# Kernel optimization log

Hardware: AMD Instinct MI355X
Metric: run time of the kernel (lower is better)

## Reference

```python
import jax, jax.numpy as jnp
import numpy as np

N_AC, N_W, D_IN = 40000, 20000, 128
H, DH, D_OUT = 4, 64, 64
E_TIC, E_W, E_REL = 400000, 200000, 400000
NEG = 0.2  # DGL GATConv leaky_relu negative slope


def _edge_softmax(e, dst, n_dst):
    # e: (E, H) edge logits; softmax over edges sharing the same dst node
    m = jax.ops.segment_max(e, dst, num_segments=n_dst)
    m = jnp.where(jnp.isfinite(m), m, 0.0)
    ex = jnp.exp(e - m[dst])
    s = jax.ops.segment_sum(ex, dst, num_segments=n_dst)
    return ex / (s[dst] + 1e-9)


def _gat(x_src, x_dst, src, dst, ew, W, al, ar, b, n_dst, act):
    # DGL GATConv (eval mode: dropouts are identity). al/ar: (H, D)
    Hh, Dd = al.shape
    z_src = (x_src @ W).reshape(-1, Hh, Dd)
    z_dst = (x_dst @ W).reshape(-1, Hh, Dd)
    el = jnp.einsum('nhd,hd->nh', z_src, al)
    er = jnp.einsum('nhd,hd->nh', z_dst, ar)
    e = jax.nn.leaky_relu(el[src] + er[dst], NEG)              # (E, H)
    a = _edge_softmax(e, dst, n_dst) * ew[:, None]             # attention * edge_weight
    out = jax.ops.segment_sum(z_src[src] * a[:, :, None], dst, num_segments=n_dst)
    out = out + b.reshape(1, Hh, Dd)
    return act(out) if act is not None else out


def _forward(x_ac, x_w, w_tic, w_w, w_rel,
             W1_tic, al1_tic, ar1_tic, b1_tic,
             W1_w, al1_w, ar1_w, b1_w,
             W1_rel, al1_rel, ar1_rel, b1_rel,
             W2_tic, al2_tic, ar2_tic, b2_tic,
             W2_w, al2_w, ar2_w, b2_w,
             W2_rel, al2_rel, ar2_rel, b2_rel,
             src_tic, dst_tic, src_w, dst_w, src_rel, dst_rel):
    elu = jax.nn.elu
    # --- layer 1 (H=4 heads, ELU activation inside GATConv) ---
    h_tic = _gat(x_ac, x_ac, src_tic, dst_tic, w_tic, W1_tic, al1_tic, ar1_tic, b1_tic, N_AC, elu)
    h_w1 = _gat(x_w, x_w, src_w, dst_w, w_w, W1_w, al1_w, ar1_w, b1_w, N_W, elu)
    h_rel = _gat(x_ac, x_w, src_rel, dst_rel, w_rel, W1_rel, al1_rel, ar1_rel, b1_rel, N_W, elu)
    # HeteroGraphConv aggregate='mean' over etypes per dst node type, flatten heads, ReLU
    h_ac = jax.nn.relu(h_tic.reshape(N_AC, -1))
    h_word = jax.nn.relu(((h_w1 + h_rel) * 0.5).reshape(N_W, -1))
    # --- layer 2 (single head, no activation) ---
    o_tic = _gat(h_ac, h_ac, src_tic, dst_tic, w_tic, W2_tic, al2_tic, ar2_tic, b2_tic, N_AC, None)
    o_w = _gat(h_word, h_word, src_w, dst_w, w_w, W2_w, al2_w, ar2_w, b2_w, N_W, None)
    o_rel = _gat(h_ac, h_word, src_rel, dst_rel, w_rel, W2_rel, al2_rel, ar2_rel, b2_rel, N_W, None)
    return (o_tic.reshape(N_AC, -1), ((o_w + o_rel) * 0.5).reshape(N_W, -1))


def setup_inputs() -> dict:
    key = jax.random.key(0)
    ks = iter(jax.random.split(key, 48))
    def p(shape):
        return jax.random.normal(next(ks), shape, jnp.float32) * 0.05
    inp = {
        'x_ac': jax.random.normal(next(ks), (N_AC, D_IN), jnp.float32),
        'x_w': jax.random.normal(next(ks), (N_W, D_IN), jnp.float32),
        'w_tic': jax.random.uniform(next(ks), (E_TIC,), jnp.float32),
        'w_w': jax.random.uniform(next(ks), (E_W,), jnp.float32),
        'w_rel': jax.random.uniform(next(ks), (E_REL,), jnp.float32),
    }
    # per-etype GATConv params: layer1 (H heads), layer2 (1 head)
    for name, fin, h, d in [('1_tic', D_IN, H, DH), ('1_w', D_IN, H, DH), ('1_rel', D_IN, H, DH),
                            ('2_tic', H * DH, 1, D_OUT), ('2_w', H * DH, 1, D_OUT), ('2_rel', H * DH, 1, D_OUT)]:
        inp['W' + name] = p((fin, h * d))
        inp['al' + name] = p((h, d))
        inp['ar' + name] = p((h, d))
        inp['b' + name] = p((h * d,))
    inp['src_tic'] = jax.random.randint(next(ks), (E_TIC,), 0, N_AC, jnp.int32)
    inp['dst_tic'] = jax.random.randint(next(ks), (E_TIC,), 0, N_AC, jnp.int32)
    inp['src_w'] = jax.random.randint(next(ks), (E_W,), 0, N_W, jnp.int32)
    inp['dst_w'] = jax.random.randint(next(ks), (E_W,), 0, N_W, jnp.int32)
    inp['src_rel'] = jax.random.randint(next(ks), (E_REL,), 0, N_AC, jnp.int32)
    inp['dst_rel'] = jax.random.randint(next(ks), (E_REL,), 0, N_W, jnp.int32)
    return inp


def reference(x_ac, x_w, w_tic, w_w, w_rel,
              W1_tic, al1_tic, ar1_tic, b1_tic,
              W1_w, al1_w, ar1_w, b1_w,
              W1_rel, al1_rel, ar1_rel, b1_rel,
              W2_tic, al2_tic, ar2_tic, b2_tic,
              W2_w, al2_w, ar2_w, b2_w,
              W2_rel, al2_rel, ar2_rel, b2_rel,
              src_tic, dst_tic, src_w, dst_w, src_rel, dst_rel):
    return _forward(x_ac, x_w, w_tic, w_w, w_rel,
                    W1_tic, al1_tic, ar1_tic, b1_tic,
                    W1_w, al1_w, ar1_w, b1_w,
                    W1_rel, al1_rel, ar1_rel, b1_rel,
                    W2_tic, al2_tic, ar2_tic, b2_tic,
                    W2_w, al2_w, ar2_w, b2_w,
                    W2_rel, al2_rel, ar2_rel, b2_rel,
                    src_tic, dst_tic, src_w, dst_w, src_rel, dst_rel)
```

## Files before the change

### kernel.cpp

```cpp
#include <hip/hip_runtime.h>
#include <hip/hip_bf16.h>

typedef unsigned short ushort_t;
typedef __attribute__((ext_vector_type(8))) short bf16x8;
typedef __attribute__((ext_vector_type(4))) float f32x4;

#define N_AC 40000
#define N_W  20000
#define D_IN 128
#define NH   4
#define HD   256
#define DOUT 64
#define E_TIC 400000
#define E_W   200000
#define E_REL 400000
#define E_ALL 1000000
#define N_ALL 80000
#define NEG 0.2f
#define CAP 96
#define FCH 4096
#define ELLW 64

__device__ __forceinline__ float bf2f(ushort_t u) {
    return __uint_as_float(((unsigned int)u) << 16);
}
__device__ __forceinline__ ushort_t f2bf(float v) {
    unsigned u = __float_as_uint(v);
    unsigned r = (u + 0x7fffu + ((u >> 16) & 1u)) >> 16;
    return (ushort_t)r;
}
__device__ __forceinline__ float ldf(const void* p, size_t i, int f) {
    return f ? ((const float*)p)[i] : bf2f(((const ushort_t*)p)[i]);
}
__device__ __forceinline__ float lrelu_exp(float v) {
    v = v > 0.f ? v : NEG * v;
    return __expf(v);
}

__global__ void detect_dtype(const ushort_t* __restrict__ x, int* __restrict__ flag) {
    __shared__ int hit;
    if (threadIdx.x == 0) hit = 0;
    __syncthreads();
    for (int i = threadIdx.x; i < 4096; i += 256) {
        float v = bf2f(x[i]);
        if (!(fabsf(v) <= 1e4f)) atomicOr(&hit, 1);
    }
    __syncthreads();
    if (threadIdx.x == 0) flag[0] = hit ? 1 : 0;
}

struct CvtTab { const void* src[24]; int n[24]; int off[24]; };
__global__ __launch_bounds__(256) void cvt_inputs(CvtTab t, float* __restrict__ par,
                                                  const int* __restrict__ flagp) {
    int ent = blockIdx.x >> 3, sub = blockIdx.x & 7;
    int f = flagp[0];
    const void* s = t.src[ent];
    int n = t.n[ent];
    float* d = par + t.off[ent];
    for (int i = sub * 256 + threadIdx.x; i < n; i += 8 * 256)
        d[i] = f ? ((const float*)s)[i] : bf2f(((const ushort_t*)s)[i]);
}

struct QTab { int woff[2]; int aoff[2]; int qoff[2]; int K[2]; int Hh[2]; };
__global__ __launch_bounds__(256) void make_q(QTab t, float* __restrict__ par) {
    int b = blockIdx.x;
    int k = threadIdx.x;
    int K = t.K[b], Hh = t.Hh[b];
    if (k >= K) return;
    const float* W = par + t.woff[b];
    const float* a = par + t.aoff[b];
    float* q = par + t.qoff[b];
    int HDc = Hh * 64;
    for (int h = 0; h < Hh; ++h) {
        float s = 0.f;
        for (int d = 0; d < 64; ++d) s += W[(size_t)k * HDc + h * 64 + d] * a[h * 64 + d];
        q[k * Hh + h] = s;
    }
}

struct PTab { int woff[6]; int toff[6]; int Klog[6]; int N[6]; };
__global__ __launch_bounds__(256) void pack_wt(PTab t, const float* __restrict__ par,
                                               ushort_t* __restrict__ wt) {
    int m = blockIdx.x >> 4, sub = blockIdx.x & 15;
    int Klog = t.Klog[m], K = 1 << Klog, Nn = t.N[m];
    int tot = K * Nn;
    const float* Wp = par + t.woff[m];
    ushort_t* d = wt + t.toff[m];
    for (int i = sub * 256 + threadIdx.x; i < tot; i += 16 * 256) {
        int n = i >> Klog, k = i & (K - 1);
        d[i] = f2bf(Wp[(size_t)k * Nn + n]);
    }
}


__device__ __forceinline__ void dev_mgemm1(int b, const void* X, int f,
                                           const ushort_t* WT, ushort_t* Zb,
                                           const float* alp, const float* arp,
                                           float* elo, float* ero) {
    const int w = threadIdx.x >> 6, l = threadIdx.x & 63;
    const int row0 = b * 16;
    const int lr = l & 15, lk = l >> 4;

    bf16x8 a[4];
    if (!f) {
        const ushort_t* xp = (const ushort_t*)X + (size_t)(row0 + lr) * 128 + lk * 8;
        #pragma unroll
        for (int ks = 0; ks < 4; ++ks) a[ks] = *(const bf16x8*)(xp + ks * 32);
    } else {
        const float* xp = (const float*)X + (size_t)(row0 + lr) * 128 + lk * 8;
        #pragma unroll
        for (int ks = 0; ks < 4; ++ks)
            #pragma unroll
            for (int j = 0; j < 8; ++j) a[ks][j] = (short)f2bf(xp[ks * 32 + j]);
    }

    f32x4 acc[4] = {{0.f,0.f,0.f,0.f},{0.f,0.f,0.f,0.f},{0.f,0.f,0.f,0.f},{0.f,0.f,0.f,0.f}};
    const int col0 = w * 64;
    #pragma unroll
    for (int ks = 0; ks < 4; ++ks) {
        #pragma unroll
        for (int nt = 0; nt < 4; ++nt) {
            bf16x8 bb = *(const bf16x8*)(WT + (size_t)(col0 + nt * 16 + lr) * 128 + ks * 32 + lk * 8);
            acc[nt] = __builtin_amdgcn_mfma_f32_16x16x32_bf16(a[ks], bb, acc[nt], 0, 0, 0);
        }
    }
    #pragma unroll
    for (int nt = 0; nt < 4; ++nt)
        #pragma unroll
        for (int r = 0; r < 4; ++r)
            Zb[(size_t)(row0 + lk * 4 + r) * HD + col0 + nt * 16 + lr] = f2bf(acc[nt][r]);

    if (alp) {
        float a0 = alp[col0 + lr], a1 = alp[col0 + 16 + lr],
              a2 = alp[col0 + 32 + lr], a3 = alp[col0 + 48 + lr];
        #pragma unroll
        for (int r = 0; r < 4; ++r) {
            float v = acc[0][r] * a0 + acc[1][r] * a1 + acc[2][r] * a2 + acc[3][r] * a3;
            v += __shfl_xor(v, 1, 64); v += __shfl_xor(v, 2, 64);
            v += __shfl_xor(v, 4, 64); v += __shfl_xor(v, 8, 64);
            if (lr == r) elo[(size_t)(row0 + lk * 4 + r) * 4 + w] = v;
        }
    }
    if (arp) {
        float a0 = arp[col0 + lr], a1 = arp[col0 + 16 + lr],
              a2 = arp[col0 + 32 + lr], a3 = arp[col0 + 48 + lr];
        #pragma unroll
        for (int r = 0; r < 4; ++r) {
            float v = acc[0][r] * a0 + acc[1][r] * a1 + acc[2][r] * a2 + acc[3][r] * a3;
            v += __shfl_xor(v, 1, 64); v += __shfl_xor(v, 2, 64);
            v += __shfl_xor(v, 4, 64); v += __shfl_xor(v, 8, 64);
            if (lr == r) ero[(size_t)(row0 + lk * 4 + r) * 4 + w] = v;
        }
    }
}

__device__ __forceinline__ void dev_fill_ell(int b,
        const int* s0, const int* d0, const void* w0,
        const int* s1, const int* d1, const void* w1,
        const int* s2, const int* d2, const void* w2,
        int f, int* cnt, unsigned* adj) {
    const int CB[9] = {0, 12500, 25000, 37500, 50000, 61250, 67500, 73750, 80000};
    const int cls = b & 7;
    const int lo = CB[cls], hi = CB[cls + 1];
    const int e0 = (b >> 3) * FCH;
    for (int i = threadIdx.x; i < FCH; i += 256) {
        int e = e0 + i;
        if (e >= E_ALL) return;
        int g;
        if (e < E_TIC) g = d0[e];
        else if (e < E_TIC + E_W) g = N_AC + d1[e - E_TIC];
        else g = N_AC + N_W + d2[e - E_TIC - E_W];
        if (g < lo || g >= hi) continue;
        int sn; float ew;
        if (e < E_TIC) { sn = s0[e]; ew = ldf(w0, e, f); }
        else if (e < E_TIC + E_W) { int le = e - E_TIC; sn = s1[le]; ew = ldf(w1, le, f); }
        else { int le = e - E_TIC - E_W; sn = s2[le]; ew = ldf(w2, le, f); }
        int r = atomicAdd(&cnt[g], 1);
        if (r < ELLW)
            adj[(size_t)g * ELLW + r] = (unsigned)(sn & 0xFFFF) | ((unsigned)f2bf(ew) << 16);
    }
}

__device__ __forceinline__ void dev_elr1(int b, const void* X, int f,
                                         const float* q0, float* o0,
                                         int N, int D, int Hh) {
    __shared__ float qs[512];
    const int tid = threadIdx.x;
    const int tot = D * Hh;
    for (int i = tid; i < tot; i += 256) {
        int k, h;
        if (Hh == 4) { k = i >> 2; h = i & 3; } else { k = i; h = 0; }
        qs[h * D + k] = q0[i];
    }
    __syncthreads();
    const int wid = tid >> 6, lane = tid & 63;
    const int n = b * 4 + wid;
    if (n >= N) return;
    const int J = D >> 6;
    float x[4];
    for (int j = 0; j < J; ++j) x[j] = ldf(X, (size_t)n * D + j * 64 + lane, f);
    for (int h = 0; h < Hh; ++h) {
        float v = 0.f;
        for (int j = 0; j < J; ++j) v += x[j] * qs[h * D + j * 64 + lane];
        #pragma unroll
        for (int o = 32; o > 0; o >>= 1) v += __shfl_down(v, o, 64);
        if (lane == 0) o0[n * Hh + h] = v;
    }
}

struct FA {
    const int *s0, *d0; const void* w0;
    const int *s1, *d1; const void* w1;
    const int *s2, *d2; const void* w2;
    const int* flagp; int* cnt; unsigned* adj;
    const void* x_ac; const void* x_w;
    const ushort_t *WTt, *WTw, *WTr;
    ushort_t *Zt, *Zw, *Zr;
    const float *al1t, *ar1t, *al1w, *ar1w, *al1r;
    float *ELt, *ERt, *ELw, *ERw, *ELr, *ERr;
    const float* qer1r;
    unsigned c0, c1, c2, c3;
};
__global__ __launch_bounds__(256) void fused_a(FA a) {
    const unsigned b = blockIdx.x;
    const int f = a.flagp[0];
    if (b < a.c0) {
        dev_fill_ell(b, a.s0, a.d0, a.w0, a.s1, a.d1, a.w1, a.s2, a.d2, a.w2,
                     f, a.cnt, a.adj);
    } else if (b < a.c1) {
        dev_mgemm1(b - a.c0, a.x_ac, f, a.WTt, a.Zt, a.al1t, a.ar1t, a.ELt, a.ERt);
    } else if (b < a.c2) {
        dev_mgemm1(b - a.c1, a.x_w, f, a.WTw, a.Zw, a.al1w, a.ar1w, a.ELw, a.ERw);
    } else if (b < a.c3) {
        dev_mgemm1(b - a.c2, a.x_ac, f, a.WTr, a.Zr, a.al1r, nullptr, a.ELr, nullptr);
    } else {
        dev_elr1(b - a.c3, a.x_w, f, a.qer1r, a.ERr, N_W, 128, 4);
    }
}

__global__ __launch_bounds__(256) void count3(const int* __restrict__ d0,
                                              const int* __restrict__ d1,
                                              const int* __restrict__ d2,
                                              int* __restrict__ cnt,
                                              int* __restrict__ rank) {
    int e = blockIdx.x * 256 + threadIdx.x;
    if (e >= E_ALL) return;
    int g;
    if (e < E_TIC) g = d0[e];
    else if (e < E_TIC + E_W) g = N_AC + d1[e - E_TIC];
    else g = N_AC + N_W + d2[e - E_TIC - E_W];
    rank[e] = atomicAdd(&cnt[g], 1);
}

__global__ __launch_bounds__(256) void scan_bsum(const int* __restrict__ cnt,
                                                 int* __restrict__ bsum, int N) {
    __shared__ int red[256];
    int i = blockIdx.x * 256 + threadIdx.x;
    red[threadIdx.x] = (i < N) ? cnt[i] : 0;
    __syncthreads();
    #pragma unroll
    for (int o = 128; o > 0; o >>= 1) {
        if (threadIdx.x < o) red[threadIdx.x] += red[threadIdx.x + o];
        __syncthreads();
    }
    if (threadIdx.x == 0) bsum[blockIdx.x] = red[0];
}

__global__ __launch_bounds__(512) void scan_top(int* __restrict__ bsum, int B) {
    __shared__ int sc[512];
    const int t = threadIdx.x;
    int v = (t < B) ? bsum[t] : 0;
    sc[t] = v;
    __syncthreads();
    #pragma unroll
    for (int o = 1; o < 512; o <<= 1) {
        int u = (t >= o) ? sc[t - o] : 0;
        __syncthreads();
        sc[t] += u;
        __syncthreads();
    }
    if (t < B) bsum[t] = sc[t] - v;
}

__global__ __launch_bounds__(256) void scan_out(const int* __restrict__ cnt,
                                                const int* __restrict__ bsum,
                                                int* __restrict__ rowptr, int N) {
    __shared__ int sc[256];
    const int t = threadIdx.x;
    int i = blockIdx.x * 256 + t;
    int v = (i < N) ? cnt[i] : 0;
    sc[t] = v;
    __syncthreads();
    #pragma unroll
    for (int o = 1; o < 256; o <<= 1) {
        int u = (t >= o) ? sc[t - o] : 0;
        __syncthreads();
        sc[t] += u;
        __syncthreads();
    }
    int ex = sc[t] - v + bsum[blockIdx.x];
    if (i < N) {
        rowptr[i] = ex;
        if (i == N - 1) rowptr[N] = ex + v;
    }
}

__global__ __launch_bounds__(256) void fill3(const int* __restrict__ s0, const int* __restrict__ d0, const void* __restrict__ w0,
                                             const int* __restrict__ s1, const int* __restrict__ d1, const void* __restrict__ w1,
                                             const int* __restrict__ s2, const int* __restrict__ d2, const void* __restrict__ w2,
                                             const int* __restrict__ flagp,
                                             const int* __restrict__ rp,
                                             const int* __restrict__ rank,
                                             unsigned* __restrict__ adj) {
    const int CB[9] = {0, 12500, 25000, 37500, 50000, 61250, 67500, 73750, 80000};
    const int cls = blockIdx.x & 7;
    const int lo = CB[cls], hi = CB[cls + 1];
    const int f = flagp[0];
    const int e0 = (blockIdx.x >> 3) * FCH;
    for (int i = threadIdx.x; i < FCH; i += 256) {
        int e = e0 + i;
        if (e >= E_ALL) return;
        int g;
        if (e < E_TIC) g = d0[e];
        else if (e < E_TIC + E_W) g = N_AC + d1[e - E_TIC];
        else g = N_AC + N_W + d2[e - E_TIC - E_W];
        if (g < lo || g >= hi) continue;
        int sn; float ew;
        if (e < E_TIC) { sn = s0[e]; ew = ldf(w0, e, f); }
        else if (e < E_TIC + E_W) { int le = e - E_TIC; sn = s1[le]; ew = ldf(w1, le, f); }
        else { int le = e - E_TIC - E_W; sn = s2[le]; ew = ldf(w2, le, f); }
        int pos = rp[g] + rank[e];
        adj[pos] = (unsigned)(sn & 0xFFFF) | ((unsigned)f2bf(ew) << 16);
    }
}

__global__ __launch_bounds__(256) void mgemm1(const void* __restrict__ X,
                                              const int* __restrict__ flagp,
                                              const ushort_t* __restrict__ WT,
                                              ushort_t* __restrict__ Zb,
                                              const float* __restrict__ alp,
                                              const float* __restrict__ arp,
                                              float* __restrict__ elo,
                                              float* __restrict__ ero) {
    dev_mgemm1(blockIdx.x, X, flagp[0], WT, Zb, alp, arp, elo, ero);
}

__global__ __launch_bounds__(256) void elr1(const void* __restrict__ X,
                                            const int* __restrict__ flagp,
                                            const float* __restrict__ q0,
                                            float* __restrict__ o0,
                                            int N, int D, int Hh) {
    dev_elr1(blockIdx.x, X, flagp ? flagp[0] : 0, q0, o0, N, D, Hh);
}

struct G2 {
    const ushort_t* Hb[3]; const ushort_t* WT[3]; ushort_t* Zc[3];
    const float* al[3]; const float* ar[3]; float* el[3]; float* er[3];
    int N[3]; int b1, b2;
};
__global__ __launch_bounds__(256) void mgemm2_all(G2 t) {
    int s, b;
    if (blockIdx.x < (unsigned)t.b1) { s = 0; b = blockIdx.x; }
    else if (blockIdx.x < (unsigned)t.b2) { s = 1; b = blockIdx.x - t.b1; }
    else { s = 2; b = blockIdx.x - t.b2; }
    const int w = threadIdx.x >> 6, l = threadIdx.x & 63;
    const int row0 = b * 64 + w * 16;
    if (row0 >= t.N[s]) return;
    const int lr = l & 15, lk = l >> 4;
    const ushort_t* ap = t.Hb[s] + (size_t)(row0 + lr) * 256 + lk * 8;
    const ushort_t* WT = t.WT[s];

    f32x4 acc[4] = {{0.f,0.f,0.f,0.f},{0.f,0.f,0.f,0.f},{0.f,0.f,0.f,0.f},{0.f,0.f,0.f,0.f}};
    #pragma unroll
    for (int ks = 0; ks < 8; ++ks) {
        bf16x8 a = *(const bf16x8*)(ap + ks * 32);
        #pragma unroll
        for (int nt = 0; nt < 4; ++nt) {
            bf16x8 bb = *(const bf16x8*)(WT + (size_t)(nt * 16 + lr) * 256 + ks * 32 + lk * 8);
            acc[nt] = __builtin_amdgcn_mfma_f32_16x16x32_bf16(a, bb, acc[nt], 0, 0, 0);
        }
    }
    ushort_t* Zc = t.Zc[s];
    #pragma unroll
    for (int nt = 0; nt < 4; ++nt)
        #pragma unroll
        for (int r = 0; r < 4; ++r)
            Zc[(size_t)(row0 + lk * 4 + r) * DOUT + nt * 16 + lr] = f2bf(acc[nt][r]);

    if (t.al[s]) {
        const float* alp = t.al[s];
        float a0 = alp[lr], a1 = alp[16 + lr], a2 = alp[32 + lr], a3 = alp[48 + lr];
        #pragma unroll
        for (int r = 0; r < 4; ++r) {
            float v = acc[0][r] * a0 + acc[1][r] * a1 + acc[2][r] * a2 + acc[3][r] * a3;
            v += __shfl_xor(v, 1, 64); v += __shfl_xor(v, 2, 64);
            v += __shfl_xor(v, 4, 64); v += __shfl_xor(v, 8, 64);
            if (lr == r) t.el[s][row0 + lk * 4 + r] = v;
        }
    }
    if (t.ar[s]) {
        const float* arp = t.ar[s];
        float a0 = arp[lr], a1 = arp[16 + lr], a2 = arp[32 + lr], a3 = arp[48 + lr];
        #pragma unroll
        for (int r = 0; r < 4; ++r) {
            float v = acc[0][r] * a0 + acc[1][r] * a1 + acc[2][r] * a2 + acc[3][r] * a3;
            v += __shfl_xor(v, 1, 64); v += __shfl_xor(v, 2, 64);
            v += __shfl_xor(v, 4, 64); v += __shfl_xor(v, 8, 64);
            if (lr == r) t.er[s][row0 + lk * 4 + r] = v;
        }
    }
}

template <int MODE>
__global__ __launch_bounds__(256) void gat1(const int* __restrict__ rp,
                                            const int* __restrict__ degp,
                                            int gbase, int ell,
                                            const unsigned* __restrict__ adj,
                                            const ushort_t* __restrict__ zb,
                                            const float* __restrict__ el,
                                            const float* __restrict__ er,
                                            const float* __restrict__ bias,
                                            ushort_t* __restrict__ H, int N) {
    __shared__ float atl[4][CAP * 4];
    __shared__ int   snl[4][CAP];
    const int w = threadIdx.x >> 6, lane = threadIdx.x & 63;
    const int n = blockIdx.x * 4 + w;
    if (n >= N) return;
    const int h = lane >> 4;
    int beg, deg;
    if (ell) {
        int g = gbase + n;
        beg = g * ELLW;
        deg = degp[g];
        deg = deg < ELLW ? deg : ELLW;
    } else {
        beg = rp[n];
        deg = rp[n + 1] - beg;
    }
    const float4* el4 = (const float4*)el;
    const float4 ern = ((const float4*)er)[n];

    float4 ss = make_float4(0.f, 0.f, 0.f, 0.f);
    for (int base = 0; base < deg; base += 64) {
        int i = base + lane;
        if (i < deg) {
            unsigned ae = adj[beg + i];
            int sn = ae & 0xFFFF;
            float4 e = el4[sn];
            float x0 = lrelu_exp(e.x + ern.x);
            float x1 = lrelu_exp(e.y + ern.y);
            float x2 = lrelu_exp(e.z + ern.z);
            float x3 = lrelu_exp(e.w + ern.w);
            ss.x += x0; ss.y += x1; ss.z += x2; ss.w += x3;
            if (i < CAP) {
                float ew = bf2f((ushort_t)(ae >> 16));
                float4* dst4 = (float4*)&atl[w][i * 4];
                *dst4 = make_float4(x0 * ew, x1 * ew, x2 * ew, x3 * ew);
                snl[w][i] = sn;
            }
        }
    }
    #pragma unroll
    for (int o = 32; o > 0; o >>= 1) {
        ss.x += __shfl_xor(ss.x, o, 64);
        ss.y += __shfl_xor(ss.y, o, 64);
        ss.z += __shfl_xor(ss.z, o, 64);
        ss.w += __shfl_xor(ss.w, o, 64);
    }
    const float sh = (h == 0) ? ss.x : (h == 1) ? ss.y : (h == 2) ? ss.z : ss.w;
    const float inv = 1.f / (sh + 1e-9f);
    const float erh = (h == 0) ? ern.x : (h == 1) ? ern.y : (h == 2) ? ern.z : ern.w;

    float a0 = 0.f, a1 = 0.f, a2 = 0.f, a3 = 0.f;
    #pragma unroll 4
    for (int i = 0; i < deg; ++i) {
        int sn; float atv;
        if (i < CAP) {
            sn = snl[w][i];
            atv = atl[w][i * 4 + h];
        } else {
            unsigned ae = adj[beg + i];
            sn = ae & 0xFFFF;
            atv = lrelu_exp(el[sn * 4 + h] + erh) * bf2f((ushort_t)(ae >> 16));
        }
        ushort4 zv = *(const ushort4*)(zb + (size_t)sn * HD + lane * 4);
        a0 += bf2f(zv.x) * atv; a1 += bf2f(zv.y) * atv;
        a2 += bf2f(zv.z) * atv; a3 += bf2f(zv.w) * atv;
    }
    float4 b = *(const float4*)(bias + lane * 4);
    a0 = a0 * inv + b.x; a1 = a1 * inv + b.y;
    a2 = a2 * inv + b.z; a3 = a3 * inv + b.w;

    ushort_t* hp = H + (size_t)n * HD + lane * 4;
    ushort4 o;
    if (MODE == 0) {
        o.x = f2bf(a0 > 0.f ? a0 : 0.f); o.y = f2bf(a1 > 0.f ? a1 : 0.f);
        o.z = f2bf(a2 > 0.f ? a2 : 0.f); o.w = f2bf(a3 > 0.f ? a3 : 0.f);
    } else if (MODE == 1) {
        o.x = f2bf(a0 > 0.f ? a0 : expm1f(a0)); o.y = f2bf(a1 > 0.f ? a1 : expm1f(a1));
        o.z = f2bf(a2 > 0.f ? a2 : expm1f(a2)); o.w = f2bf(a3 > 0.f ? a3 : expm1f(a3));
    } else {
        ushort4 hw = *(const ushort4*)hp;
        float v0 = (bf2f(hw.x) + (a0 > 0.f ? a0 : expm1f(a0))) * 0.5f;
        float v1 = (bf2f(hw.y) + (a1 > 0.f ? a1 : expm1f(a1))) * 0.5f;
        float v2 = (bf2f(hw.z) + (a2 > 0.f ? a2 : expm1f(a2))) * 0.5f;
        float v3 = (bf2f(hw.w) + (a3 > 0.f ? a3 : expm1f(a3))) * 0.5f;
        o.x = f2bf(v0 > 0.f ? v0 : 0.f); o.y = f2bf(v1 > 0.f ? v1 : 0.f);
        o.z = f2bf(v2 > 0.f ? v2 : 0.f); o.w = f2bf(v3 > 0.f ? v3 : 0.f);
    }
    *(ushort4*)hp = o;
}

struct GA2 {
    const int* rp[3]; const int* degp; int gbase[3]; int ell;
    const ushort_t* zc[3]; const float* el[3]; const float* er[3];
    int N[3]; int b1, b2;
};
__global__ __launch_bounds__(256) void gat2_all(GA2 t, const unsigned* __restrict__ adj,
                                                const float* __restrict__ b2t,
                                                float* __restrict__ ACCw,
                                                float* __restrict__ ACCr,
                                                void* __restrict__ out,
                                                const int* __restrict__ flagp) {
    __shared__ float atl[4][CAP];
    __shared__ int   snl[4][CAP];
    int s, b;
    if (blockIdx.x < (unsigned)t.b1) { s = 0; b = blockIdx.x; }
    else if (blockIdx.x < (unsigned)t.b2) { s = 1; b = blockIdx.x - t.b1; }
    else { s = 2; b = blockIdx.x - t.b2; }
    const int w = threadIdx.x >> 6, lane = threadIdx.x & 63;
    const int n = b * 4 + w;
    if (n >= t.N[s]) return;
    const float* el = t.el[s];
    const ushort_t* zb = t.zc[s];
    int beg, deg;
    if (t.ell) {
        int g = t.gbase[s] + n;
        beg = g * ELLW;
        deg = t.degp[g];
        deg = deg < ELLW ? deg : ELLW;
    } else {
        const int* rp = t.rp[s];
        beg = rp[n];
        deg = rp[n + 1] - beg;
    }
    const float ern = t.er[s][n];

    float ssum = 0.f;
    for (int base = 0; base < deg; base += 64) {
        int i = base + lane;
        if (i < deg) {
            unsigned ae = adj[beg + i];
            int sn = ae & 0xFFFF;
            float x = lrelu_exp(el[sn] + ern);
            ssum += x;
            if (i < CAP) {
                atl[w][i] = x * bf2f((ushort_t)(ae >> 16));
                snl[w][i] = sn;
            }
        }
    }
    #pragma unroll
    for (int o = 32; o > 0; o >>= 1) ssum += __shfl_xor(ssum, o, 64);
    const float inv = 1.f / (ssum + 1e-9f);

    const int eoff = lane >> 4;
    const int c4 = (lane & 15) * 4;
    const int degc = deg < CAP ? deg : CAP;
    float a0 = 0.f, a1 = 0.f, a2 = 0.f, a3 = 0.f;
    #pragma unroll 2
    for (int i = 0; i < degc; i += 4) {
        int ii = i + eoff;
        int iic = ii < degc ? ii : degc - 1;
        float atv = ii < degc ? atl[w][iic] : 0.f;
        int sn = snl[w][iic];
        ushort4 zv = *(const ushort4*)(zb + (size_t)sn * DOUT + c4);
        a0 += bf2f(zv.x) * atv; a1 += bf2f(zv.y) * atv;
        a2 += bf2f(zv.z) * atv; a3 += bf2f(zv.w) * atv;
    }
    for (int i = CAP; i < deg; i += 4) {
        int ii = i + eoff;
        int iic = ii < deg ? ii : deg - 1;
        unsigned ae = adj[beg + iic];
        int sn = ae & 0xFFFF;
        float atv = lrelu_exp(el[sn] + ern) * bf2f((ushort_t)(ae >> 16));
        if (ii >= deg) atv = 0.f;
        ushort4 zv = *(const ushort4*)(zb + (size_t)sn * DOUT + c4);
        a0 += bf2f(zv.x) * atv; a1 += bf2f(zv.y) * atv;
        a2 += bf2f(zv.z) * atv; a3 += bf2f(zv.w) * atv;
    }
    a0 += __shfl_xor(a0, 16, 64); a0 += __shfl_xor(a0, 32, 64);
    a1 += __shfl_xor(a1, 16, 64); a1 += __shfl_xor(a1, 32, 64);
    a2 += __shfl_xor(a2, 16, 64); a2 += __shfl_xor(a2, 32, 64);
    a3 += __shfl_xor(a3, 16, 64); a3 += __shfl_xor(a3, 32, 64);
    a0 *= inv; a1 *= inv; a2 *= inv; a3 *= inv;

    if (lane < 16) {
        size_t o = (size_t)n * DOUT + c4;
        if (s == 0) {
            float v0 = a0 + b2t[c4], v1 = a1 + b2t[c4 + 1];
            float v2 = a2 + b2t[c4 + 2], v3 = a3 + b2t[c4 + 3];
            if (flagp[0]) { *(float4*)((float*)out + o) = make_float4(v0, v1, v2, v3); }
            else {
                ushort4 ov;
                ov.x = f2bf(v0); ov.y = f2bf(v1); ov.z = f2bf(v2); ov.w = f2bf(v3);
                *(ushort4*)((ushort_t*)out + o) = ov;
            }
        } else if (s == 1) {
            *(float4*)(ACCw + o) = make_float4(a0, a1, a2, a3);
        } else {
            *(float4*)(ACCr + o) = make_float4(a0, a1, a2, a3);
        }
    }
}

__global__ __launch_bounds__(256) void out_word(const float* __restrict__ aw,
                                                const float* __restrict__ bw,
                                                const float* __restrict__ ar_,
                                                const float* __restrict__ br,
                                                void* __restrict__ out,
                                                const int* __restrict__ flagp, int total) {
    int i = blockIdx.x * 256 + threadIdx.x;
    if (i >= total) return;
    int c = i & 63;
    float v = ((aw[i] + bw[c]) + (ar_[i] + br[c])) * 0.5f;
    size_t o = (size_t)N_AC * DOUT + i;
    if (flagp[0]) ((float*)out)[o] = v;
    else ((ushort_t*)out)[o] = f2bf(v);
}

extern "C" void kernel_launch(void* const* d_in, const int* in_sizes, int n_in,
                              void* d_out, int out_size, void* d_ws, size_t ws_size,
                              hipStream_t stream) {
    (void)in_sizes; (void)n_in; (void)out_size;

    const void* x_ac = d_in[0];
    const void* x_w  = d_in[1];
    const void* ew_tic = d_in[2];
    const void* ew_w   = d_in[3];
    const void* ew_rel = d_in[4];
    const int* src_tic = (const int*)d_in[29];
    const int* dst_tic = (const int*)d_in[30];
    const int* src_w   = (const int*)d_in[31];
    const int* dst_w   = (const int*)d_in[32];
    const int* src_rel = (const int*)d_in[33];
    const int* dst_rel = (const int*)d_in[34];

    float* ws = (float*)d_ws;
    int* FLAG = (int*)ws;

    float* PAR = ws + 16;
    const int o_W1t = 1000000, o_W1w = 1032768, o_W1r = 1065536;
    const int o_W2t = 1098304, o_W2w = 1114688, o_W2r = 1131072;
    const int o_al1t = 1147456, o_ar1t = 1147712, o_al1w = 1147968, o_ar1w = 1148224,
              o_al1r = 1148480, o_ar1r = 1148736;
    const int o_b1t = 1148992, o_b1w = 1149248, o_b1r = 1149504;
    const int o_al2t = 1149760, o_ar2t = 1149824, o_al2w = 1149888, o_ar2w = 1149952,
              o_al2r = 1150016, o_ar2r = 1150080;
    const int o_b2t = 1150144, o_b2w = 1150208, o_b2r = 1150272;
    const int o_qer1r = 1150400, o_qer2r = 1150912;

    float* EB   = ws + 1160016;
    float* ELt  = EB;
    float* ERt  = EB + 160000;
    float* ELw  = EB + 320000;
    float* ERw  = EB + 400000;
    float* ELr  = EB + 480000;
    float* ERr  = EB + 640000;
    float* E2tl = EB + 720000;
    float* E2tr = EB + 760000;
    float* E2wl = EB + 800000;
    float* E2wr = EB + 820000;
    float* E2rl = EB + 840000;
    float* E2rr = EB + 880000;

    const size_t NEED_A = 27813744ull * 4ull;
    const bool pathA = ws_size >= NEED_A;

    detect_dtype<<<1, 256, 0, stream>>>((const ushort_t*)x_ac, FLAG);

    CvtTab ct;
    const int srcIdx[24] = {5,6,7,8, 9,10,11,12, 13,14,15,16,
                            17,18,19,20, 21,22,23,24, 25,26,27,28};
    const int sizes[24] = {32768,256,256,256, 32768,256,256,256, 32768,256,256,256,
                           16384,64,64,64, 16384,64,64,64, 16384,64,64,64};
    const int offs[24] = {o_W1t,o_al1t,o_ar1t,o_b1t, o_W1w,o_al1w,o_ar1w,o_b1w,
                          o_W1r,o_al1r,o_ar1r,o_b1r,
                          o_W2t,o_al2t,o_ar2t,o_b2t, o_W2w,o_al2w,o_ar2w,o_b2w,
                          o_W2r,o_al2r,o_ar2r,o_b2r};
    for (int i = 0; i < 24; ++i) { ct.src[i] = d_in[srcIdx[i]]; ct.n[i] = sizes[i]; ct.off[i] = offs[i]; }
    cvt_inputs<<<24 * 8, 256, 0, stream>>>(ct, PAR, FLAG);

    QTab qt;
    qt.woff[0] = o_W1r; qt.aoff[0] = o_ar1r; qt.qoff[0] = o_qer1r; qt.K[0] = 128; qt.Hh[0] = 4;
    qt.woff[1] = o_W2r; qt.aoff[1] = o_ar2r; qt.qoff[1] = o_qer2r; qt.K[1] = 256; qt.Hh[1] = 1;
    make_q<<<2, 256, 0, stream>>>(qt, PAR);

    if (pathA) {
        ushort_t* Z_tic = (ushort_t*)(ws + 2060016);
        ushort_t* Z_w   = (ushort_t*)(ws + 7180016);
        ushort_t* Z_rel = (ushort_t*)(ws + 9740016);
        float* ACCw = ws + 9740016;
        float* ACCr = ws + 11020016;
        ushort_t* Hac = (ushort_t*)(ws + 14860016);
        ushort_t* Hw  = (ushort_t*)(ws + 19980016);
        ushort_t* WT  = (ushort_t*)(ws + 22540016);
        int* cntA = (int*)(ws + 22613744);
        unsigned* adjA = (unsigned*)(ws + 22693744);
        ushort_t* Zc_tic = Z_tic;
        ushort_t* Zc_w   = Z_tic + 2560000;
        ushort_t* Zc_r   = Z_tic + 3840000;
        const int t_W1t = 0, t_W1w = 32768, t_W1r = 65536,
                  t_W2t = 98304, t_W2w = 114688, t_W2r = 131072;

        PTab pt;
        const int pw[6] = {o_W1t, o_W1w, o_W1r, o_W2t, o_W2w, o_W2r};
        const int ptf[6] = {t_W1t, t_W1w, t_W1r, t_W2t, t_W2w, t_W2r};
        for (int i = 0; i < 6; ++i) {
            pt.woff[i] = pw[i]; pt.toff[i] = ptf[i];
            pt.Klog[i] = (i < 3) ? 7 : 8; pt.N[i] = (i < 3) ? 256 : 64;
        }
        pack_wt<<<6 * 16, 256, 0, stream>>>(pt, PAR, WT);

        hipMemsetAsync(cntA, 0, N_ALL * 4, stream);

        FA fa;
        fa.s0 = src_tic; fa.d0 = dst_tic; fa.w0 = ew_tic;
        fa.s1 = src_w;   fa.d1 = dst_w;   fa.w1 = ew_w;
        fa.s2 = src_rel; fa.d2 = dst_rel; fa.w2 = ew_rel;
        fa.flagp = FLAG; fa.cnt = cntA; fa.adj = adjA;
        fa.x_ac = x_ac; fa.x_w = x_w;
        fa.WTt = WT + t_W1t; fa.WTw = WT + t_W1w; fa.WTr = WT + t_W1r;
        fa.Zt = Z_tic; fa.Zw = Z_w; fa.Zr = Z_rel;
        fa.al1t = PAR + o_al1t; fa.ar1t = PAR + o_ar1t;
        fa.al1w = PAR + o_al1w; fa.ar1w = PAR + o_ar1w;
        fa.al1r = PAR + o_al1r;
        fa.ELt = ELt; fa.ERt = ERt; fa.ELw = ELw; fa.ERw = ERw;
        fa.ELr = ELr; fa.ERr = ERr;
        fa.qer1r = PAR + o_qer1r;
        const unsigned nf = 8 * ((E_ALL + FCH - 1) / FCH);
        fa.c0 = nf;
        fa.c1 = fa.c0 + N_AC / 16;
        fa.c2 = fa.c1 + N_W / 16;
        fa.c3 = fa.c2 + N_AC / 16;
        const unsigned ctot = fa.c3 + N_W / 4;
        fused_a<<<ctot, 256, 0, stream>>>(fa);

        gat1<0><<<N_AC / 4, 256, 0, stream>>>(nullptr, cntA, 0, 1, adjA, Z_tic,
                                              ELt, ERt, PAR + o_b1t, Hac, N_AC);
        gat1<1><<<N_W / 4, 256, 0, stream>>>(nullptr, cntA, N_AC, 1, adjA, Z_w,
                                             ELw, ERw, PAR + o_b1w, Hw, N_W);
        gat1<2><<<N_W / 4, 256, 0, stream>>>(nullptr, cntA, N_AC + N_W, 1, adjA, Z_rel,
                                             ELr, ERr, PAR + o_b1r, Hw, N_W);

        elr1<<<N_W / 4, 256, 0, stream>>>(Hw, nullptr, PAR + o_qer2r, E2rr, N_W, 256, 1);

        G2 g2;
        g2.Hb[0] = Hac; g2.Hb[1] = Hw; g2.Hb[2] = Hac;
        g2.WT[0] = WT + t_W2t; g2.WT[1] = WT + t_W2w; g2.WT[2] = WT + t_W2r;
        g2.Zc[0] = Zc_tic; g2.Zc[1] = Zc_w; g2.Zc[2] = Zc_r;
        g2.al[0] = PAR + o_al2t; g2.al[1] = PAR + o_al2w; g2.al[2] = PAR + o_al2r;
        g2.ar[0] = PAR + o_ar2t; g2.ar[1] = PAR + o_ar2w; g2.ar[2] = nullptr;
        g2.el[0] = E2tl; g2.el[1] = E2wl; g2.el[2] = E2rl;
        g2.er[0] = E2tr; g2.er[1] = E2wr; g2.er[2] = nullptr;
        g2.N[0] = N_AC; g2.N[1] = N_W; g2.N[2] = N_AC;
        const int nb0 = (N_AC + 63) / 64, nb1 = (N_W + 63) / 64, nb2 = (N_AC + 63) / 64;
        g2.b1 = nb0; g2.b2 = nb0 + nb1;
        mgemm2_all<<<nb0 + nb1 + nb2, 256, 0, stream>>>(g2);

        GA2 ga;
        ga.rp[0] = ga.rp[1] = ga.rp[2] = nullptr;
        ga.degp = cntA; ga.ell = 1;
        ga.gbase[0] = 0; ga.gbase[1] = N_AC; ga.gbase[2] = N_AC + N_W;
        ga.zc[0] = Zc_tic; ga.zc[1] = Zc_w; ga.zc[2] = Zc_r;
        ga.el[0] = E2tl; ga.el[1] = E2wl; ga.el[2] = E2rl;
        ga.er[0] = E2tr; ga.er[1] = E2wr; ga.er[2] = E2rr;
        ga.N[0] = N_AC; ga.N[1] = N_W; ga.N[2] = N_W;
        const int gb0 = N_AC / 4, gb1 = N_W / 4, gb2 = N_W / 4;
        ga.b1 = gb0; ga.b2 = gb0 + gb1;
        gat2_all<<<gb0 + gb1 + gb2, 256, 0, stream>>>(ga, adjA, PAR + o_b2t, ACCw, ACCr, d_out, FLAG);

        out_word<<<(N_W * DOUT) / 256, 256, 0, stream>>>(ACCw, PAR + o_b2w, ACCr, PAR + o_b2r,
                                                         d_out, FLAG, N_W * DOUT);
    } else {
        float* ACC = ws + 2060016;
        ushort_t* Zb  = (ushort_t*)(ws + 3340016);
        ushort_t* Hac = (ushort_t*)(ws + 8460016);
        ushort_t* Hw  = (ushort_t*)(ws + 13580016);
        ushort_t* WT  = (ushort_t*)(ws + 16140016);
        const int t_W1t = 0, t_W1w = 32768, t_W1r = 65536,
                  t_W2t = 98304, t_W2w = 114688, t_W2r = 131072;
        int* IB = (int*)(ws + 16213760);
        int* rp   = IB;
        int* cnt  = IB + 80064;
        int* bsum = IB + 160128;
        unsigned* adj = (unsigned*)(IB + 160704);
        int* rank = IB + 1160704;
        float* ACCr = ws + 18374464;
        ushort_t* Zc_tic = Zb;
        ushort_t* Zc_w   = Zb + 2560000;
        ushort_t* Zc_r   = Zb + 3840000;

        PTab pt;
        const int pw[6] = {o_W1t, o_W1w, o_W1r, o_W2t, o_W2w, o_W2r};
        const int ptf[6] = {t_W1t, t_W1w, t_W1r, t_W2t, t_W2w, t_W2r};
        for (int i = 0; i < 6; ++i) {
            pt.woff[i] = pw[i]; pt.toff[i] = ptf[i];
            pt.Klog[i] = (i < 3) ? 7 : 8; pt.N[i] = (i < 3) ? 256 : 64;
        }
        pack_wt<<<6 * 16, 256, 0, stream>>>(pt, PAR, WT);

        {
            const int B = (N_ALL + 255) / 256;
            hipMemsetAsync(cnt, 0, N_ALL * 4, stream);
            count3<<<(E_ALL + 255) / 256, 256, 0, stream>>>(dst_tic, dst_w, dst_rel, cnt, rank);
            scan_bsum<<<B, 256, 0, stream>>>(cnt, bsum, N_ALL);
            scan_top<<<1, 512, 0, stream>>>(bsum, B);
            scan_out<<<B, 256, 0, stream>>>(cnt, bsum, rp, N_ALL);
            fill3<<<8 * ((E_ALL + FCH - 1) / FCH), 256, 0, stream>>>(
                src_tic, dst_tic, ew_tic, src_w, dst_w, ew_w, src_rel, dst_rel, ew_rel,
                FLAG, rp, rank, adj);
        }
        const int* rp_tic = rp;
        const int* rp_w   = rp + N_AC;
        const int* rp_rel = rp + N_AC + N_W;

        elr1<<<N_W / 4, 256, 0, stream>>>(x_w, FLAG, PAR + o_qer1r, ERr, N_W, 128, 4);

        mgemm1<<<N_AC / 16, 256, 0, stream>>>(x_ac, FLAG, WT + t_W1t, Zb,
                                              PAR + o_al1t, PAR + o_ar1t, ELt, ERt);
        gat1<0><<<N_AC / 4, 256, 0, stream>>>(rp_tic, nullptr, 0, 0, adj, Zb,
                                              ELt, ERt, PAR + o_b1t, Hac, N_AC);

        mgemm1<<<N_W / 16, 256, 0, stream>>>(x_w, FLAG, WT + t_W1w, Zb,
                                             PAR + o_al1w, PAR + o_ar1w, ELw, ERw);
        gat1<1><<<N_W / 4, 256, 0, stream>>>(rp_w, nullptr, 0, 0, adj, Zb,
                                             ELw, ERw, PAR + o_b1w, Hw, N_W);

        mgemm1<<<N_AC / 16, 256, 0, stream>>>(x_ac, FLAG, WT + t_W1r, Zb,
                                              PAR + o_al1r, nullptr, ELr, nullptr);
        gat1<2><<<N_W / 4, 256, 0, stream>>>(rp_rel, nullptr, 0, 0, adj, Zb,
                                             ELr, ERr, PAR + o_b1r, Hw, N_W);

        elr1<<<N_W / 4, 256, 0, stream>>>(Hw, nullptr, PAR + o_qer2r, E2rr, N_W, 256, 1);

        G2 g2;
        g2.Hb[0] = Hac; g2.Hb[1] = Hw; g2.Hb[2] = Hac;
        g2.WT[0] = WT + t_W2t; g2.WT[1] = WT + t_W2w; g2.WT[2] = WT + t_W2r;
        g2.Zc[0] = Zc_tic; g2.Zc[1] = Zc_w; g2.Zc[2] = Zc_r;
        g2.al[0] = PAR + o_al2t; g2.al[1] = PAR + o_al2w; g2.al[2] = PAR + o_al2r;
        g2.ar[0] = PAR + o_ar2t; g2.ar[1] = PAR + o_ar2w; g2.ar[2] = nullptr;
        g2.el[0] = E2tl; g2.el[1] = E2wl; g2.el[2] = E2rl;
        g2.er[0] = E2tr; g2.er[1] = E2wr; g2.er[2] = nullptr;
        g2.N[0] = N_AC; g2.N[1] = N_W; g2.N[2] = N_AC;
        const int nb0 = (N_AC + 63) / 64, nb1 = (N_W + 63) / 64, nb2 = (N_AC + 63) / 64;
        g2.b1 = nb0; g2.b2 = nb0 + nb1;
        mgemm2_all<<<nb0 + nb1 + nb2, 256, 0, stream>>>(g2);

        GA2 ga;
        ga.rp[0] = rp_tic; ga.rp[1] = rp_w; ga.rp[2] = rp_rel;
        ga.degp = nullptr; ga.ell = 0;
        ga.gbase[0] = ga.gbase[1] = ga.gbase[2] = 0;
        ga.zc[0] = Zc_tic; ga.zc[1] = Zc_w; ga.zc[2] = Zc_r;
        ga.el[0] = E2tl; ga.el[1] = E2wl; ga.el[2] = E2rl;
        ga.er[0] = E2tr; ga.er[1] = E2wr; ga.er[2] = E2rr;
        ga.N[0] = N_AC; ga.N[1] = N_W; ga.N[2] = N_W;
        const int gb0 = N_AC / 4, gb1 = N_W / 4, gb2 = N_W / 4;
        ga.b1 = gb0; ga.b2 = gb0 + gb1;
        gat2_all<<<gb0 + gb1 + gb2, 256, 0, stream>>>(ga, adj, PAR + o_b2t, ACC, ACCr, d_out, FLAG);

        out_word<<<(N_W * DOUT) / 256, 256, 0, stream>>>(ACC, PAR + o_b2w, ACCr, PAR + o_b2r,
                                                         d_out, FLAG, N_W * DOUT);
    }
}
```

Before: 341.0 us.

## Simplify ELL fill, merge tic/word gat1 launches, fuse layer-2 er projection

The ELL fill now uses one thread per edge instead of eight destination-range classes that each rescanned every edge chunk. This removes the redundant reads of the destination arrays at the cost of atomics spread across all destinations. The tic and word layer-1 aggregation kernels are merged into a single launch. The layer-2 rel er dot product is computed inside the final gat1 epilogue, which removes a separate elr1 pass over Hw.

New measurement: 349.4 us. 1.02x slower.

```diff
diff --git a/kernel.cpp b/kernel.cpp
--- a/kernel.cpp
+++ b/kernel.cpp
@@ -154,31 +154,26 @@
     }
 }
 
-__device__ __forceinline__ void dev_fill_ell(int b,
+__device__ __forceinline__ void dev_fill_ell1(int b,
         const int* s0, const int* d0, const void* w0,
         const int* s1, const int* d1, const void* w1,
         const int* s2, const int* d2, const void* w2,
         int f, int* cnt, unsigned* adj) {
-    const int CB[9] = {0, 12500, 25000, 37500, 50000, 61250, 67500, 73750, 80000};
-    const int cls = b & 7;
-    const int lo = CB[cls], hi = CB[cls + 1];
-    const int e0 = (b >> 3) * FCH;
-    for (int i = threadIdx.x; i < FCH; i += 256) {
-        int e = e0 + i;
-        if (e >= E_ALL) return;
-        int g;
-        if (e < E_TIC) g = d0[e];
-        else if (e < E_TIC + E_W) g = N_AC + d1[e - E_TIC];
-        else g = N_AC + N_W + d2[e - E_TIC - E_W];
-        if (g < lo || g >= hi) continue;
-        int sn; float ew;
-        if (e < E_TIC) { sn = s0[e]; ew = ldf(w0, e, f); }
-        else if (e < E_TIC + E_W) { int le = e - E_TIC; sn = s1[le]; ew = ldf(w1, le, f); }
-        else { int le = e - E_TIC - E_W; sn = s2[le]; ew = ldf(w2, le, f); }
-        int r = atomicAdd(&cnt[g], 1);
-        if (r < ELLW)
-            adj[(size_t)g * ELLW + r] = (unsigned)(sn & 0xFFFF) | ((unsigned)f2bf(ew) << 16);
-    }
+    int e = b * 256 + threadIdx.x;
+    if (e >= E_ALL) return;
+    int g, sn; float ew;
+    if (e < E_TIC) {
+        g = d0[e]; sn = s0[e]; ew = ldf(w0, e, f);
+    } else if (e < E_TIC + E_W) {
+        int le = e - E_TIC;
+        g = N_AC + d1[le]; sn = s1[le]; ew = ldf(w1, le, f);
+    } else {
+        int le = e - E_TIC - E_W;
+        g = N_AC + N_W + d2[le]; sn = s2[le]; ew = ldf(w2, le, f);
+    }
+    int r = atomicAdd(&cnt[g], 1);
+    if (r < ELLW)
+        adj[(size_t)g * ELLW + r] = (unsigned)(sn & 0xFFFF) | ((unsigned)f2bf(ew) << 16);
 }
 
 __device__ __forceinline__ void dev_elr1(int b, const void* X, int f,
@@ -206,6 +201,110 @@
         for (int o = 32; o > 0; o >>= 1) v += __shfl_down(v, o, 64);
         if (lane == 0) o0[n * Hh + h] = v;
     }
+}
+
+template <int MODE>
+__device__ __forceinline__ void dev_gat1(int b,
+        const int* rp, const int* degp, int gbase, int ell,
+        const unsigned* adj, const ushort_t* zb,
+        const float* el, const float* er, const float* bias,
+        ushort_t* H, int N, const float* q2, float* e2out) {
+    __shared__ float atl[4][CAP * 4];
+    __shared__ int   snl[4][CAP];
+    const int w = threadIdx.x >> 6, lane = threadIdx.x & 63;
+    const int n = b * 4 + w;
+    if (n >= N) return;
+    const int h = lane >> 4;
+    int beg, deg;
+    if (ell) {
+        int g = gbase + n;
+        beg = g * ELLW;
+        deg = degp[g];
+        deg = deg < ELLW ? deg : ELLW;
+    } else {
+        beg = rp[n];
+        deg = rp[n + 1] - beg;
+    }
+    const float4* el4 = (const float4*)el;
+    const float4 ern = ((const float4*)er)[n];
+
+    float4 ss = make_float4(0.f, 0.f, 0.f, 0.f);
+    for (int base = 0; base < deg; base += 64) {
+        int i = base + lane;
+        if (i < deg) {
+            unsigned ae = adj[beg + i];
+            int sn = ae & 0xFFFF;
+            float4 e = el4[sn];
+            float x0 = lrelu_exp(e.x + ern.x);
+            float x1 = lrelu_exp(e.y + ern.y);
+            float x2 = lrelu_exp(e.z + ern.z);
+            float x3 = lrelu_exp(e.w + ern.w);
+            ss.x += x0; ss.y += x1; ss.z += x2; ss.w += x3;
+            if (i < CAP) {
+                float ew = bf2f((ushort_t)(ae >> 16));
+                float4* dst4 = (float4*)&atl[w][i * 4];
+                *dst4 = make_float4(x0 * ew, x1 * ew, x2 * ew, x3 * ew);
+                snl[w][i] = sn;
+            }
+        }
+    }
+    #pragma unroll
+    for (int o = 32; o > 0; o >>= 1) {
+        ss.x += __shfl_xor(ss.x, o, 64);
+        ss.y += __shfl_xor(ss.y, o, 64);
+        ss.z += __shfl_xor(ss.z, o, 64);
+        ss.w += __shfl_xor(ss.w, o, 64);
+    }
+    const float sh = (h == 0) ? ss.x : (h == 1) ? ss.y : (h == 2) ? ss.z : ss.w;
+    const float inv = 1.f / (sh + 1e-9f);
+    const float erh = (h == 0) ? ern.x : (h == 1) ? ern.y : (h == 2) ? ern.z : ern.w;
+
+    float a0 = 0.f, a1 = 0.f, a2 = 0.f, a3 = 0.f;
+    #pragma unroll 4
+    for (int i = 0; i < deg; ++i) {
+        int sn; float atv;
+        if (i < CAP) {
+            sn = snl[w][i];
+            atv = atl[w][i * 4 + h];
+        } else {
+            unsigned ae = adj[beg + i];
+            sn = ae & 0xFFFF;
+            atv = lrelu_exp(el[sn * 4 + h] + erh) * bf2f((ushort_t)(ae >> 16));
+        }
+        ushort4 zv = *(const ushort4*)(zb + (size_t)sn * HD + lane * 4);
+        a0 += bf2f(zv.x) * atv; a1 += bf2f(zv.y) * atv;
+        a2 += bf2f(zv.z) * atv; a3 += bf2f(zv.w) * atv;
+    }
+    float4 bb = *(const float4*)(bias + lane * 4);
+    a0 = a0 * inv + bb.x; a1 = a1 * inv + bb.y;
+    a2 = a2 * inv + bb.z; a3 = a3 * inv + bb.w;
+
+    ushort_t* hp = H + (size_t)n * HD + lane * 4;
+    ushort4 o;
+    if (MODE == 0) {
+        o.x = f2bf(a0 > 0.f ? a0 : 0.f); o.y = f2bf(a1 > 0.f ? a1 : 0.f);
+        o.z = f2bf(a2 > 0.f ? a2 : 0.f); o.w = f2bf(a3 > 0.f ? a3 : 0.f);
+    } else if (MODE == 1) {
+        o.x = f2bf(a0 > 0.f ? a0 : expm1f(a0)); o.y = f2bf(a1 > 0.f ? a1 : expm1f(a1));
+        o.z = f2bf(a2 > 0.f ? a2 : expm1f(a2)); o.w = f2bf(a3 > 0.f ? a3 : expm1f(a3));
+    } else {
+        ushort4 hw = *(const ushort4*)hp;
+        float v0 = (bf2f(hw.x) + (a0 > 0.f ? a0 : expm1f(a0))) * 0.5f;
+        float v1 = (bf2f(hw.y) + (a1 > 0.f ? a1 : expm1f(a1))) * 0.5f;
+        float v2 = (bf2f(hw.z) + (a2 > 0.f ? a2 : expm1f(a2))) * 0.5f;
+        float v3 = (bf2f(hw.w) + (a3 > 0.f ? a3 : expm1f(a3))) * 0.5f;
+        v0 = v0 > 0.f ? v0 : 0.f; v1 = v1 > 0.f ? v1 : 0.f;
+        v2 = v2 > 0.f ? v2 : 0.f; v3 = v3 > 0.f ? v3 : 0.f;
+        o.x = f2bf(v0); o.y = f2bf(v1); o.z = f2bf(v2); o.w = f2bf(v3);
+        if (q2) {
+            const int c4 = lane * 4;
+            float d = v0 * q2[c4] + v1 * q2[c4 + 1] + v2 * q2[c4 + 2] + v3 * q2[c4 + 3];
+            #pragma unroll
+            for (int oo = 32; oo > 0; oo >>= 1) d += __shfl_xor(d, oo, 64);
+            if (lane == 0) e2out[n] = d;
+        }
+    }
+    *(ushort4*)hp = o;
 }
 
 struct FA {
@@ -225,8 +324,8 @@
     const unsigned b = blockIdx.x;
     const int f = a.flagp[0];
     if (b < a.c0) {
-        dev_fill_ell(b, a.s0, a.d0, a.w0, a.s1, a.d1, a.w1, a.s2, a.d2, a.w2,
-                     f, a.cnt, a.adj);
+        dev_fill_ell1(b, a.s0, a.d0, a.w0, a.s1, a.d1, a.w1, a.s2, a.d2, a.w2,
+                      f, a.cnt, a.adj);
     } else if (b < a.c1) {
         dev_mgemm1(b - a.c0, a.x_ac, f, a.WTt, a.Zt, a.al1t, a.ar1t, a.ELt, a.ERt);
     } else if (b < a.c2) {
@@ -236,6 +335,37 @@
     } else {
         dev_elr1(b - a.c3, a.x_w, f, a.qer1r, a.ERr, N_W, 128, 4);
     }
+}
+
+struct GT {
+    const int* degp; const unsigned* adj;
+    const ushort_t *Zt, *Zw;
+    const float *ELt, *ERt, *ELw, *ERw, *b1t, *b1w;
+    ushort_t *Hac, *Hw;
+    unsigned b1;
+};
+__global__ __launch_bounds__(256) void gat1_tw(GT t) {
+    if (blockIdx.x < t.b1)
+        dev_gat1<0>(blockIdx.x, nullptr, t.degp, 0, 1, t.adj, t.Zt,
+                    t.ELt, t.ERt, t.b1t, t.Hac, N_AC, nullptr, nullptr);
+    else
+        dev_gat1<1>(blockIdx.x - t.b1, nullptr, t.degp, N_AC, 1, t.adj, t.Zw,
+                    t.ELw, t.ERw, t.b1w, t.Hw, N_W, nullptr, nullptr);
+}
+
+template <int MODE>
+__global__ __launch_bounds__(256) void gat1(const int* __restrict__ rp,
+                                            const int* __restrict__ degp,
+                                            int gbase, int ell,
+                                            const unsigned* __restrict__ adj,
+                                            const ushort_t* __restrict__ zb,
+                                            const float* __restrict__ el,
+                                            const float* __restrict__ er,
+                                            const float* __restrict__ bias,
+                                            ushort_t* __restrict__ H, int N,
+                                            const float* __restrict__ q2,
+                                            float* __restrict__ e2out) {
+    dev_gat1<MODE>(blockIdx.x, rp, degp, gbase, ell, adj, zb, el, er, bias, H, N, q2, e2out);
 }
 
 __global__ __launch_bounds__(256) void count3(const int* __restrict__ d0,
@@ -409,106 +539,6 @@
             if (lr == r) t.er[s][row0 + lk * 4 + r] = v;
         }
     }
-}
-
-template <int MODE>
-__global__ __launch_bounds__(256) void gat1(const int* __restrict__ rp,
-                                            const int* __restrict__ degp,
-                                            int gbase, int ell,
-                                            const unsigned* __restrict__ adj,
-                                            const ushort_t* __restrict__ zb,
-                                            const float* __restrict__ el,
-                                            const float* __restrict__ er,
-                                            const float* __restrict__ bias,
-                                            ushort_t* __restrict__ H, int N) {
-    __shared__ float atl[4][CAP * 4];
-    __shared__ int   snl[4][CAP];
-    const int w = threadIdx.x >> 6, lane = threadIdx.x & 63;
-    const int n = blockIdx.x * 4 + w;
-    if (n >= N) return;
-    const int h = lane >> 4;
-    int beg, deg;
-    if (ell) {
-        int g = gbase + n;
-        beg = g * ELLW;
-        deg = degp[g];
-        deg = deg < ELLW ? deg : ELLW;
-    } else {
-        beg = rp[n];
-        deg = rp[n + 1] - beg;
-    }
-    const float4* el4 = (const float4*)el;
-    const float4 ern = ((const float4*)er)[n];
-
-    float4 ss = make_float4(0.f, 0.f, 0.f, 0.f);
-    for (int base = 0; base < deg; base += 64) {
-        int i = base + lane;
-        if (i < deg) {
-            unsigned ae = adj[beg + i];
-            int sn = ae & 0xFFFF;
-            float4 e = el4[sn];
-            float x0 = lrelu_exp(e.x + ern.x);
-            float x1 = lrelu_exp(e.y + ern.y);
-            float x2 = lrelu_exp(e.z + ern.z);
-            float x3 = lrelu_exp(e.w + ern.w);
-            ss.x += x0; ss.y += x1; ss.z += x2; ss.w += x3;
-            if (i < CAP) {
-                float ew = bf2f((ushort_t)(ae >> 16));
-                float4* dst4 = (float4*)&atl[w][i * 4];
-                *dst4 = make_float4(x0 * ew, x1 * ew, x2 * ew, x3 * ew);
-                snl[w][i] = sn;
-            }
-        }
-    }
-    #pragma unroll
-    for (int o = 32; o > 0; o >>= 1) {
-        ss.x += __shfl_xor(ss.x, o, 64);
-        ss.y += __shfl_xor(ss.y, o, 64);
-        ss.z += __shfl_xor(ss.z, o, 64);
-        ss.w += __shfl_xor(ss.w, o, 64);
-    }
-    const float sh = (h == 0) ? ss.x : (h == 1) ? ss.y : (h == 2) ? ss.z : ss.w;
-    const float inv = 1.f / (sh + 1e-9f);
-    const float erh = (h == 0) ? ern.x : (h == 1) ? ern.y : (h == 2) ? ern.z : ern.w;
-
-    float a0 = 0.f, a1 = 0.f, a2 = 0.f, a3 = 0.f;
-    #pragma unroll 4
-    for (int i = 0; i < deg; ++i) {
-        int sn; float atv;
-        if (i < CAP) {
-            sn = snl[w][i];
-            atv = atl[w][i * 4 + h];
-        } else {
-            unsigned ae = adj[beg + i];
-            sn = ae & 0xFFFF;
-            atv = lrelu_exp(el[sn * 4 + h] + erh) * bf2f((ushort_t)(ae >> 16));
-        }
-        ushort4 zv = *(const ushort4*)(zb + (size_t)sn * HD + lane * 4);
-        a0 += bf2f(zv.x) * atv; a1 += bf2f(zv.y) * atv;
-        a2 += bf2f(zv.z) * atv; a3 += bf2f(zv.w) * atv;
-    }
-    float4 b = *(const float4*)(bias + lane * 4);
-    a0 = a0 * inv + b.x; a1 = a1 * inv + b.y;
-    a2 = a2 * inv + b.z; a3 = a3 * inv + b.w;
-
-    ushort_t* hp = H + (size_t)n * HD + lane * 4;
-    ushort4 o;
-    if (MODE == 0) {
-        o.x = f2bf(a0 > 0.f ? a0 : 0.f); o.y = f2bf(a1 > 0.f ? a1 : 0.f);
-        o.z = f2bf(a2 > 0.f ? a2 : 0.f); o.w = f2bf(a3 > 0.f ? a3 : 0.f);
-    } else if (MODE == 1) {
-        o.x = f2bf(a0 > 0.f ? a0 : expm1f(a0)); o.y = f2bf(a1 > 0.f ? a1 : expm1f(a1));
-        o.z = f2bf(a2 > 0.f ? a2 : expm1f(a2)); o.w = f2bf(a3 > 0.f ? a3 : expm1f(a3));
-    } else {
-        ushort4 hw = *(const ushort4*)hp;
-        float v0 = (bf2f(hw.x) + (a0 > 0.f ? a0 : expm1f(a0))) * 0.5f;
-        float v1 = (bf2f(hw.y) + (a1 > 0.f ? a1 : expm1f(a1))) * 0.5f;
-        float v2 = (bf2f(hw.z) + (a2 > 0.f ? a2 : expm1f(a2))) * 0.5f;
-        float v3 = (bf2f(hw.w) + (a3 > 0.f ? a3 : expm1f(a3))) * 0.5f;
-        o.x = f2bf(v0 > 0.f ? v0 : 0.f); o.y = f2bf(v1 > 0.f ? v1 : 0.f);
-        o.z = f2bf(v2 > 0.f ? v2 : 0.f); o.w = f2bf(v3 > 0.f ? v3 : 0.f);
-    }
-    *(ushort4*)hp = o;
 }
 
 struct GA2 {
@@ -738,22 +768,25 @@
         fa.ELt = ELt; fa.ERt = ERt; fa.ELw = ELw; fa.ERw = ERw;
         fa.ELr = ELr; fa.ERr = ERr;
         fa.qer1r = PAR + o_qer1r;
-        const unsigned nf = 8 * ((E_ALL + FCH - 1) / FCH);
-        fa.c0 = nf;
+        fa.c0 = (E_ALL + 255) / 256;
         fa.c1 = fa.c0 + N_AC / 16;
         fa.c2 = fa.c1 + N_W / 16;
         fa.c3 = fa.c2 + N_AC / 16;
         const unsigned ctot = fa.c3 + N_W / 4;
         fused_a<<<ctot, 256, 0, stream>>>(fa);
 
-        gat1<0><<<N_AC / 4, 256, 0, stream>>>(nullptr, cntA, 0, 1, adjA, Z_tic,
-                                              ELt, ERt, PAR + o_b1t, Hac, N_AC);
-        gat1<1><<<N_W / 4, 256, 0, stream>>>(nullptr, cntA, N_AC, 1, adjA, Z_w,
-                                             ELw, ERw, PAR + o_b1w, Hw, N_W);
+        GT gt;
+        gt.degp = cntA; gt.adj = adjA;
+        gt.Zt = Z_tic; gt.Zw = Z_w;
+        gt.ELt = ELt; gt.ERt = ERt; gt.ELw = ELw; gt.ERw = ERw;
+        gt.b1t = PAR + o_b1t; gt.b1w = PAR + o_b1w;
+        gt.Hac = Hac; gt.Hw = Hw;
+        gt.b1 = N_AC / 4;
+        gat1_tw<<<N_AC / 4 + N_W / 4, 256, 0, stream>>>(gt);
+
         gat1<2><<<N_W / 4, 256, 0, stream>>>(nullptr, cntA, N_AC + N_W, 1, adjA, Z_rel,
-                                             ELr, ERr, PAR + o_b1r, Hw, N_W);
-
-        elr1<<<N_W / 4, 256, 0, stream>>>(Hw, nullptr, PAR + o_qer2r, E2rr, N_W, 256, 1);
+                                             ELr, ERr, PAR + o_b1r, Hw, N_W,
+                                             PAR + o_qer2r, E2rr);
 
         G2 g2;
         g2.Hb[0] = Hac; g2.Hb[1] = Hw; g2.Hb[2] = Hac;
@@ -830,17 +863,17 @@
         mgemm1<<<N_AC / 16, 256, 0, stream>>>(x_ac, FLAG, WT + t_W1t, Zb,
                                               PAR + o_al1t, PAR + o_ar1t, ELt, ERt);
         gat1<0><<<N_AC / 4, 256, 0, stream>>>(rp_tic, nullptr, 0, 0, adj, Zb,
-                                              ELt, ERt, PAR + o_b1t, Hac, N_AC);
+                                              ELt, ERt, PAR + o_b1t, Hac, N_AC, nullptr, nullptr);
 
         mgemm1<<<N_W / 16, 256, 0, stream>>>(x_w, FLAG, WT + t_W1w, Zb,
                                              PAR + o_al1w, PAR + o_ar1w, ELw, ERw);
         gat1<1><<<N_W / 4, 256, 0, stream>>>(rp_w, nullptr, 0, 0, adj, Zb,
-                                             ELw, ERw, PAR + o_b1w, Hw, N_W);
+                                             ELw, ERw, PAR + o_b1w, Hw, N_W, nullptr, nullptr);
 
         mgemm1<<<N_AC / 16, 256, 0, stream>>>(x_ac, FLAG, WT + t_W1r, Zb,
                                               PAR + o_al1r, nullptr, ELr, nullptr);
         gat1<2><<<N_W / 4, 256, 0, stream>>>(rp_rel, nullptr, 0, 0, adj, Zb,
-                                             ELr, ERr, PAR + o_b1r, Hw, N_W);
+                                             ELr, ERr, PAR + o_b1r, Hw, N_W, nullptr, nullptr);
 
         elr1<<<N_W / 4, 256, 0, stream>>>(Hw, nullptr, PAR + o_qer2r, E2rr, N_W, 256, 1);
 
```
